# Performance work log

Measured on AMD Instinct MI355X. Metric: run time of the kernel, lower is better.

## Reference

```python
import jax, jax.numpy as jnp
import numpy as np

K = 4096      # kmer_num = 4^k with k=6
C = 10        # class_num
D = 128       # embedding dim
B = 1000      # batch of reads
L = 512       # kmers per read


def setup_inputs() -> dict:
    key = jax.random.key(0)
    k1, k2, k3, k4, k5 = jax.random.split(key, 5)
    u = jax.random.uniform(k1, (K, K))
    pair_counts = jnp.where(u > 0.9, jnp.floor(u * 50.0), 0.0).astype(jnp.float32)
    pair_counts = pair_counts * (1.0 - jnp.eye(K, dtype=jnp.float32))
    reads = jax.random.randint(k2, (B, L), 0, K, dtype=jnp.int32)
    read_labels = jax.random.randint(k3, (B,), 0, C, dtype=jnp.int32)
    embs = 2.0 * jax.random.uniform(k4, (K, D), dtype=jnp.float32) - 1.0
    softmax_weights = 2.0 * jax.random.uniform(k5, (C, D), dtype=jnp.float32) - 1.0
    delta = jnp.float32(0.5)
    return {"pair_counts": pair_counts, "reads": reads, "read_labels": read_labels,
            "delta": delta, "embs": embs, "softmax_weights": softmax_weights}


def reference(pair_counts, reads, read_labels, delta, embs, softmax_weights):
    # ---- supervised term: per-read bincount -> weighted emb sum -> log_softmax ----
    # counts[b, kmer] = number of occurrences of kmer in read b (batched bincount)
    counts = jnp.zeros((B, K), dtype=jnp.float32).at[
        jnp.arange(B)[:, None], reads].add(1.0)
    read_emb = counts @ embs                              # [B, D]
    logits = read_emb @ softmax_weights.T                 # [B, C]
    logp = jax.nn.log_softmax(logits, axis=1)             # [B, C]
    supervised = -jnp.sum(logp[jnp.arange(B), read_labels])

    # ---- unsupervised term: pairwise embedding distances over nonzero pairs ----
    sqn = jnp.sum(embs * embs, axis=1)                    # [K]
    sq = sqn[:, None] + sqn[None, :] - 2.0 * (embs @ embs.T)
    sq = jnp.maximum(sq, 0.0)                             # [K, K]
    mask = pair_counts != 0
    dist = jnp.sqrt(jnp.where(mask, sq, 1.0))             # safe sqrt off-edges
    rate = jnp.exp(-dist)
    # degrees * log(rate) - rate, with log(rate) = -dist, summed over nonzero pairs
    term = jnp.where(mask, -pair_counts * dist - rate, 0.0)
    scale = 1.0 / (np.float32(K) * np.float32(K))         # 1 / 4^(2k)
    unsupervised = -jnp.sum(term) * scale

    return delta * supervised + (1.0 - delta) * unsupervised
```

## Files before the change

kernel.cpp:

```cpp
#include <hip/hip_runtime.h>
#include <hip/hip_bf16.h>

#define KN 4096
#define CN 10
#define DN 128
#define BN 1000
#define LN 512
#define UB 4096

typedef float f32x4 __attribute__((ext_vector_type(4)));
typedef short bf16x8 __attribute__((ext_vector_type(8)));

__device__ __forceinline__ short bf16bits(float x) {
    __hip_bfloat16 h = __float2bfloat16(x);
    return *reinterpret_cast<short*>(&h);
}
__device__ __forceinline__ void gload_lds16(const float* g, void* l) {
    __builtin_amdgcn_global_load_lds(
        (const __attribute__((address_space(1))) void*)g,
        (__attribute__((address_space(3))) void*)l, 16, 0, 0);
}

__global__ __launch_bounds__(256) void w2v_prep(const float* __restrict__ embs,
                                                const float* __restrict__ W,
                                                float* __restrict__ sqn,
                                                short* __restrict__ ebf,
                                                float* __restrict__ P) {
    int blk = blockIdx.x, t = threadIdx.x;
    if (blk < 512) {
        int row = t >> 5, lane = t & 31;
        int r = blk * 8 + row;
        float4 v = ((const float4*)embs)[r * 32 + lane];
        short4 s4;
        s4.x = bf16bits(v.x); s4.y = bf16bits(v.y);
        s4.z = bf16bits(v.z); s4.w = bf16bits(v.w);
        ((short4*)ebf)[r * 32 + lane] = s4;
        float ss = v.x * v.x + v.y * v.y + v.z * v.z + v.w * v.w;
        #pragma unroll
        for (int m = 16; m >= 1; m >>= 1) ss += __shfl_xor(ss, m, 64);
        if (lane == 0) sqn[r] = ss;
        return;
    }
    int pb = blk - 512;
    int r = pb * 64 + (t >> 2);
    int q = t & 3;
    const float4* er = (const float4*)(embs + (size_t)r * DN) + q * 8;
    const float4* w4 = (const float4*)W;
    float s[CN];
    #pragma unroll
    for (int c = 0; c < CN; ++c) s[c] = 0.f;
    #pragma unroll
    for (int d4 = 0; d4 < 8; ++d4) {
        float4 e = er[d4];
        #pragma unroll
        for (int c = 0; c < CN; ++c) {
            float4 w = w4[c * 32 + q * 8 + d4];
            s[c] += e.x * w.x + e.y * w.y + e.z * w.z + e.w * w.w;
        }
    }
    #pragma unroll
    for (int c = 0; c < CN; ++c) {
        s[c] += __shfl_xor(s[c], 1, 64);
        s[c] += __shfl_xor(s[c], 2, 64);
    }
    if (q == 0) {
        float* pr = P + (size_t)r * 12;
        #pragma unroll
        for (int c = 0; c < CN; ++c) pr[c] = s[c];
        pr[10] = 0.f; pr[11] = 0.f;
    }
}

__global__ __launch_bounds__(64) void w2v_main(const short* __restrict__ ebf,
                                               const float* __restrict__ sqn,
                                               const float* __restrict__ pc,
                                               const float* __restrict__ P,
                                               const int* __restrict__ reads,
                                               const int* __restrict__ labels,
                                               float* __restrict__ psup,
                                               float* __restrict__ puns) {
    __shared__ char pcT[16 * 1040];
    int blk = blockIdx.x, t = threadIdx.x;

    if (blk < UB) {
        int i0 = (blk >> 5) * 32;
        int j0 = (blk & 31) * 128;
        int lr = t & 15, lg = t >> 4;

        const short* Arow = ebf + (size_t)(i0 + lr) * DN;
        const short* Brow = ebf + (size_t)(j0 + lr) * DN;

        f32x4 acc4[2][8];
        #pragma unroll
        for (int mi = 0; mi < 2; ++mi)
            #pragma unroll
            for (int nj = 0; nj < 8; ++nj)
                acc4[mi][nj] = (f32x4){0.f, 0.f, 0.f, 0.f};

        #pragma unroll
        for (int kk = 0; kk < 4; ++kk) {
            int ko = kk * 32 + lg * 8;
            bf16x8 a0 = *(const bf16x8*)(Arow + ko);
            bf16x8 a1 = *(const bf16x8*)(Arow + (size_t)16 * DN + ko);
            bf16x8 bfr[8];
            #pragma unroll
            for (int nj = 0; nj < 8; ++nj)
                bfr[nj] = *(const bf16x8*)(Brow + (size_t)nj * 16 * DN + ko);
            #pragma unroll
            for (int nj = 0; nj < 8; ++nj) {
                acc4[0][nj] = __builtin_amdgcn_mfma_f32_16x16x32_bf16(
                    a0, bfr[nj], acc4[0][nj], 0, 0, 0);
                acc4[1][nj] = __builtin_amdgcn_mfma_f32_16x16x32_bf16(
                    a1, bfr[nj], acc4[1][nj], 0, 0, 0);
            }
        }
        __builtin_amdgcn_sched_barrier(0);

        float siv[8], sjv[8];
        #pragma unroll
        for (int mi = 0; mi < 2; ++mi)
            #pragma unroll
            for (int v = 0; v < 4; ++v)
                siv[mi * 4 + v] = sqn[i0 + mi * 16 + lg * 4 + v];
        #pragma unroll
        for (int nj = 0; nj < 8; ++nj) sjv[nj] = sqn[j0 + nj * 16 + lr];
        __builtin_amdgcn_sched_barrier(0);

        int rsub = t >> 5, csub = t & 31;
        #pragma unroll
        for (int p = 0; p < 16; ++p) {
            const float* src = pc + (size_t)(i0 + 2 * p + rsub) * KN + j0 + csub * 4;
            gload_lds16(src, pcT + p * 1040);
        }
        __builtin_amdgcn_sched_barrier(0);

        float part = 0.f;
        #pragma unroll
        for (int mi = 0; mi < 2; ++mi) {
            if (mi == 0) { asm volatile("s_waitcnt vmcnt(8)" ::: "memory"); }
            else         { asm volatile("s_waitcnt vmcnt(0)" ::: "memory"); }
            __builtin_amdgcn_sched_barrier(0);
            #pragma unroll
            for (int v = 0; v < 4; ++v) {
                int row = mi * 16 + lg * 4 + v;
                const float* prow =
                    (const float*)(pcT + (row >> 1) * 1040 + (row & 1) * 512);
                float si = siv[mi * 4 + v];
                #pragma unroll
                for (int nj = 0; nj < 8; ++nj) {
                    float pp = prow[nj * 16 + lr];
                    float sq = fmaxf(si + sjv[nj] - 2.f * acc4[mi][nj][v], 0.f);
                    float dd = sqrtf(sq);
                    float tt = fmaf(pp, dd, __expf(-dd));
                    part += (pp != 0.f) ? tt : 0.f;
                }
            }
        }
        #pragma unroll
        for (int off = 32; off > 0; off >>= 1) part += __shfl_down(part, off, 64);
        if (t == 0) puns[blk] = part;
        return;
    }

    int b = blk - UB;
    const int4* rr = (const int4*)(reads + (size_t)b * LN);
    int4 r0 = rr[t * 2], r1 = rr[t * 2 + 1];
    int idx[8] = { r0.x, r0.y, r0.z, r0.w, r1.x, r1.y, r1.z, r1.w };
    const float4* P4 = (const float4*)P;
    float s[12];
    #pragma unroll
    for (int i = 0; i < 12; ++i) s[i] = 0.f;
    #pragma unroll
    for (int k = 0; k < 8; ++k) {
        size_t o = (size_t)idx[k] * 3;
        float4 x = P4[o], y = P4[o + 1], z = P4[o + 2];
        s[0] += x.x; s[1] += x.y; s[2]  += x.z; s[3]  += x.w;
        s[4] += y.x; s[5] += y.y; s[6]  += y.z; s[7]  += y.w;
        s[8] += z.x; s[9] += z.y; s[10] += z.z; s[11] += z.w;
    }
    #pragma unroll
    for (int off = 32; off > 0; off >>= 1)
        #pragma unroll
        for (int i = 0; i < CN; ++i) s[i] += __shfl_down(s[i], off, 64);
    if (t == 0) {
        float m = s[0];
        #pragma unroll
        for (int c = 1; c < CN; ++c) m = fmaxf(m, s[c]);
        float se = 0.f;
        #pragma unroll
        for (int c = 0; c < CN; ++c) se += __expf(s[c] - m);
        float lse = m + __logf(se);
        psup[b] = -(s[labels[b]] - lse);
    }
}

__global__ __launch_bounds__(256) void w2v_final(const float* __restrict__ psup,
                                                 const float* __restrict__ puns,
                                                 const float* __restrict__ delta,
                                                 float* __restrict__ out) {
    __shared__ float r1[4], r2[4];
    int t = threadIdx.x;
    float a = 0.f, bsum = 0.f;
    for (int i = t; i < BN; i += 256)   a += psup[i];
    for (int i = t; i < UB; i += 256)   bsum += puns[i];
    #pragma unroll
    for (int off = 32; off > 0; off >>= 1) {
        a += __shfl_down(a, off, 64);
        bsum += __shfl_down(bsum, off, 64);
    }
    int lane = t & 63, wave = t >> 6;
    if (lane == 0) { r1[wave] = a; r2[wave] = bsum; }
    __syncthreads();
    if (t == 0) {
        float sup = (r1[0] + r1[1]) + (r1[2] + r1[3]);
        float uns = ((r2[0] + r2[1]) + (r2[2] + r2[3])) * (1.f / 16777216.f);
        float d = delta[0];
        out[0] = d * sup + (1.f - d) * uns;
    }
}

extern "C" void kernel_launch(void* const* d_in, const int* in_sizes, int n_in,
                              void* d_out, int out_size, void* d_ws, size_t ws_size,
                              hipStream_t stream) {
    const float* pc     = (const float*)d_in[0];
    const int*   reads  = (const int*)  d_in[1];
    const int*   labels = (const int*)  d_in[2];
    const float* delta  = (const float*)d_in[3];
    const float* embs   = (const float*)d_in[4];
    const float* W      = (const float*)d_in[5];
    float* out = (float*)d_out;

    char* ws = (char*)d_ws;
    float* sqn  = (float*)ws;
    float* P    = (float*)(ws + 16384);
    short* ebf  = (short*)(ws + 212992);
    float* psup = (float*)(ws + 1261568);
    float* puns = (float*)(ws + 1265664);

    w2v_prep<<<576, 256, 0, stream>>>(embs, W, sqn, ebf, P);
    w2v_main<<<UB + BN, 64, 0, stream>>>(ebf, sqn, pc, P, reads, labels, psup, puns);
    w2v_final<<<1, 256, 0, stream>>>(psup, puns, delta, out);
}
```

Before: 56.08 us.

## Make pair-distance blocks persistent over column chunks with triple-buffered LDS prefetch

Each unsupervised block now keeps its 32-row A fragments in registers and loops over 16 column chunks of 64 instead of handling one 32x128 tile. The pair_counts tiles stream into LDS through a three-buffer rotation with an XOR swizzle, so the next loads overlap the MFMA and epilogue work. The aim is to cut block count and launch/tail overhead, reuse A across chunks, and hide global-memory latency. The cost is fewer blocks (512) and less parallelism to hide latency, and the chunk loop now runs serially within each block.

```diff
diff --git a/kernel.cpp b/kernel.cpp
--- a/kernel.cpp
+++ b/kernel.cpp
@@ -6,7 +6,7 @@
 #define DN 128
 #define BN 1000
 #define LN 512
-#define UB 4096
+#define UB2 512
 
 typedef float f32x4 __attribute__((ext_vector_type(4)));
 typedef short bf16x8 __attribute__((ext_vector_type(8)));
@@ -79,82 +79,111 @@
                                                const int* __restrict__ labels,
                                                float* __restrict__ psup,
                                                float* __restrict__ puns) {
-    __shared__ char pcT[16 * 1040];
+    __shared__ char buf0[8192], buf1[8192], buf2[8192];
     int blk = blockIdx.x, t = threadIdx.x;
 
-    if (blk < UB) {
-        int i0 = (blk >> 5) * 32;
-        int j0 = (blk & 31) * 128;
+    if (blk < UB2) {
+        int i0 = (blk >> 2) * 32;
+        int jb = (blk & 3) * 1024;
         int lr = t & 15, lg = t >> 4;
-
-        const short* Arow = ebf + (size_t)(i0 + lr) * DN;
-        const short* Brow = ebf + (size_t)(j0 + lr) * DN;
-
-        f32x4 acc4[2][8];
-        #pragma unroll
-        for (int mi = 0; mi < 2; ++mi)
-            #pragma unroll
-            for (int nj = 0; nj < 8; ++nj)
-                acc4[mi][nj] = (f32x4){0.f, 0.f, 0.f, 0.f};
-
+        int drow = t >> 4;
+        int dcol = (t & 15) * 4;
+
+        const short* Ar = ebf + (size_t)(i0 + lr) * DN;
+        bf16x8 afr[4][2];
         #pragma unroll
         for (int kk = 0; kk < 4; ++kk) {
-            int ko = kk * 32 + lg * 8;
-            bf16x8 a0 = *(const bf16x8*)(Arow + ko);
-            bf16x8 a1 = *(const bf16x8*)(Arow + (size_t)16 * DN + ko);
-            bf16x8 bfr[8];
-            #pragma unroll
-            for (int nj = 0; nj < 8; ++nj)
-                bfr[nj] = *(const bf16x8*)(Brow + (size_t)nj * 16 * DN + ko);
-            #pragma unroll
-            for (int nj = 0; nj < 8; ++nj) {
-                acc4[0][nj] = __builtin_amdgcn_mfma_f32_16x16x32_bf16(
-                    a0, bfr[nj], acc4[0][nj], 0, 0, 0);
-                acc4[1][nj] = __builtin_amdgcn_mfma_f32_16x16x32_bf16(
-                    a1, bfr[nj], acc4[1][nj], 0, 0, 0);
-            }
-        }
-        __builtin_amdgcn_sched_barrier(0);
-
-        float siv[8], sjv[8];
+            afr[kk][0] = *(const bf16x8*)(Ar + kk * 32 + lg * 8);
+            afr[kk][1] = *(const bf16x8*)(Ar + 16 * DN + kk * 32 + lg * 8);
+        }
+        float siv[8];
         #pragma unroll
         for (int mi = 0; mi < 2; ++mi)
             #pragma unroll
             for (int v = 0; v < 4; ++v)
                 siv[mi * 4 + v] = sqn[i0 + mi * 16 + lg * 4 + v];
-        #pragma unroll
-        for (int nj = 0; nj < 8; ++nj) sjv[nj] = sqn[j0 + nj * 16 + lr];
         __builtin_amdgcn_sched_barrier(0);
 
-        int rsub = t >> 5, csub = t & 31;
-        #pragma unroll
-        for (int p = 0; p < 16; ++p) {
-            const float* src = pc + (size_t)(i0 + 2 * p + rsub) * KN + j0 + csub * 4;
-            gload_lds16(src, pcT + p * 1040);
+        char* d0 = buf0; char* d1 = buf1; char* d2 = buf2;
+        #pragma unroll
+        for (int p = 0; p < 8; ++p) {
+            const float* s0 = pc + (size_t)(i0 + 4 * p + drow) * KN + jb
+                              + (dcol ^ ((p & 3) << 3));
+            gload_lds16(s0, d0 + p * 1024);
+        }
+        #pragma unroll
+        for (int p = 0; p < 8; ++p) {
+            const float* s1 = pc + (size_t)(i0 + 4 * p + drow) * KN + jb + 64
+                              + (dcol ^ ((p & 3) << 3));
+            gload_lds16(s1, d1 + p * 1024);
         }
         __builtin_amdgcn_sched_barrier(0);
 
         float part = 0.f;
-        #pragma unroll
-        for (int mi = 0; mi < 2; ++mi) {
-            if (mi == 0) { asm volatile("s_waitcnt vmcnt(8)" ::: "memory"); }
-            else         { asm volatile("s_waitcnt vmcnt(0)" ::: "memory"); }
-            __builtin_amdgcn_sched_barrier(0);
-            #pragma unroll
-            for (int v = 0; v < 4; ++v) {
-                int row = mi * 16 + lg * 4 + v;
-                const float* prow =
-                    (const float*)(pcT + (row >> 1) * 1040 + (row & 1) * 512);
-                float si = siv[mi * 4 + v];
-                #pragma unroll
-                for (int nj = 0; nj < 8; ++nj) {
-                    float pp = prow[nj * 16 + lr];
-                    float sq = fmaxf(si + sjv[nj] - 2.f * acc4[mi][nj][v], 0.f);
-                    float dd = sqrtf(sq);
-                    float tt = fmaf(pp, dd, __expf(-dd));
-                    part += (pp != 0.f) ? tt : 0.f;
+        for (int c = 0; c < 16; ++c) {
+            __builtin_amdgcn_sched_barrier(0);
+            int jc = jb + c * 64;
+            float sjv[4];
+            #pragma unroll
+            for (int nj = 0; nj < 4; ++nj) sjv[nj] = sqn[jc + nj * 16 + lr];
+            const short* Br = ebf + (size_t)(jc + lr) * DN;
+            bf16x8 bfr[4][4];
+            #pragma unroll
+            for (int kk = 0; kk < 4; ++kk)
+                #pragma unroll
+                for (int nj = 0; nj < 4; ++nj)
+                    bfr[kk][nj] = *(const bf16x8*)(Br + (size_t)nj * 16 * DN
+                                                   + kk * 32 + lg * 8);
+            __builtin_amdgcn_sched_barrier(0);
+            if (c < 14) {
+                int j2 = jc + 128;
+                #pragma unroll
+                for (int p = 0; p < 8; ++p) {
+                    const float* sp = pc + (size_t)(i0 + 4 * p + drow) * KN + j2
+                                      + (dcol ^ ((p & 3) << 3));
+                    gload_lds16(sp, d2 + p * 1024);
                 }
             }
+            __builtin_amdgcn_sched_barrier(0);
+            if (c < 14) { asm volatile("s_waitcnt vmcnt(8)" ::: "memory"); }
+            else        { asm volatile("s_waitcnt vmcnt(0)" ::: "memory"); }
+            __builtin_amdgcn_sched_barrier(0);
+
+            f32x4 acc[2][4];
+            #pragma unroll
+            for (int mi = 0; mi < 2; ++mi)
+                #pragma unroll
+                for (int nj = 0; nj < 4; ++nj)
+                    acc[mi][nj] = (f32x4){0.f, 0.f, 0.f, 0.f};
+            #pragma unroll
+            for (int kk = 0; kk < 4; ++kk)
+                #pragma unroll
+                for (int nj = 0; nj < 4; ++nj) {
+                    acc[0][nj] = __builtin_amdgcn_mfma_f32_16x16x32_bf16(
+                        afr[kk][0], bfr[kk][nj], acc[0][nj], 0, 0, 0);
+                    acc[1][nj] = __builtin_amdgcn_mfma_f32_16x16x32_bf16(
+                        afr[kk][1], bfr[kk][nj], acc[1][nj], 0, 0, 0);
+                }
+
+            #pragma unroll
+            for (int mi = 0; mi < 2; ++mi) {
+                #pragma unroll
+                for (int v = 0; v < 4; ++v) {
+                    int row = mi * 16 + lg * 4 + v;
+                    const char* rowp = d0 + row * 256;
+                    float si = siv[mi * 4 + v];
+                    #pragma unroll
+                    for (int nj = 0; nj < 4; ++nj) {
+                        float pp = *(const float*)(rowp +
+                                     ((nj * 64 + lr * 4) ^ (lg << 5)));
+                        float sq = fmaxf(si + sjv[nj] - 2.f * acc[mi][nj][v], 0.f);
+                        float dd = sqrtf(sq);
+                        float tt = fmaf(pp, dd, __expf(-dd));
+                        part += (pp != 0.f) ? tt : 0.f;
+                    }
+                }
+            }
+            char* tmp = d0; d0 = d1; d1 = d2; d2 = tmp;
         }
         #pragma unroll
         for (int off = 32; off > 0; off >>= 1) part += __shfl_down(part, off, 64);
@@ -162,7 +191,7 @@
         return;
     }
 
-    int b = blk - UB;
+    int b = blk - UB2;
     const int4* rr = (const int4*)(reads + (size_t)b * LN);
     int4 r0 = rr[t * 2], r1 = rr[t * 2 + 1];
     int idx[8] = { r0.x, r0.y, r0.z, r0.w, r1.x, r1.y, r1.z, r1.w };
@@ -202,7 +231,7 @@
     int t = threadIdx.x;
     float a = 0.f, bsum = 0.f;
     for (int i = t; i < BN; i += 256)   a += psup[i];
-    for (int i = t; i < UB; i += 256)   bsum += puns[i];
+    for (int i = t; i < UB2; i += 256)  bsum += puns[i];
     #pragma unroll
     for (int off = 32; off > 0; off >>= 1) {
         a += __shfl_down(a, off, 64);
@@ -238,6 +267,6 @@
     float* puns = (float*)(ws + 1265664);
 
     w2v_prep<<<576, 256, 0, stream>>>(embs, W, sqn, ebf, P);
-    w2v_main<<<UB + BN, 64, 0, stream>>>(ebf, sqn, pc, P, reads, labels, psup, puns);
+    w2v_main<<<UB2 + BN, 64, 0, stream>>>(ebf, sqn, pc, P, reads, labels, psup, puns);
     w2v_final<<<1, 256, 0, stream>>>(psup, puns, delta, out);
 }
```

After: 72.55 us. +29.4%, slower.

## Split fused gram+pair kernel into bf16 distance-matrix pass and streaming reduction

Applied to the files above, without the earlier changes.

Replaces the fused kernel, which computed 32x128 gram tiles and loaded pair counts into LDS, with two kernels. The first computes 128x128 gram tiles with 4 waves and writes sqrt distances to a bf16 K×K workspace matrix. The second streams pair_counts and the distance matrix with wide coalesced loads, applies the masked term, and shares its launch with the supervised per-read blocks. The split decouples MFMA work from the pair_counts stream, but adds a 32 MB write and read of the distance matrix, an extra launch, and bf16 rounding of the distances.

```diff
diff --git a/kernel.cpp b/kernel.cpp
--- a/kernel.cpp
+++ b/kernel.cpp
@@ -6,7 +6,7 @@
 #define DN 128
 #define BN 1000
 #define LN 512
-#define UB 4096
+#define SB 2048
 
 typedef float f32x4 __attribute__((ext_vector_type(4)));
 typedef short bf16x8 __attribute__((ext_vector_type(8)));
@@ -15,10 +15,13 @@
     __hip_bfloat16 h = __float2bfloat16(x);
     return *reinterpret_cast<short*>(&h);
 }
-__device__ __forceinline__ void gload_lds16(const float* g, void* l) {
-    __builtin_amdgcn_global_load_lds(
-        (const __attribute__((address_space(1))) void*)g,
-        (__attribute__((address_space(3))) void*)l, 16, 0, 0);
+__device__ __forceinline__ float bflo(unsigned u) {
+    unsigned v = u << 16;
+    return *reinterpret_cast<float*>(&v);
+}
+__device__ __forceinline__ float bfhi(unsigned u) {
+    unsigned v = u & 0xFFFF0000u;
+    return *reinterpret_cast<float*>(&v);
 }
 
 __global__ __launch_bounds__(256) void w2v_prep(const float* __restrict__ embs,
@@ -71,98 +74,128 @@
     }
 }
 
-__global__ __launch_bounds__(64) void w2v_main(const short* __restrict__ ebf,
-                                               const float* __restrict__ sqn,
-                                               const float* __restrict__ pc,
-                                               const float* __restrict__ P,
-                                               const int* __restrict__ reads,
-                                               const int* __restrict__ labels,
-                                               float* __restrict__ psup,
-                                               float* __restrict__ puns) {
-    __shared__ char pcT[16 * 1040];
+__global__ __launch_bounds__(256, 4) void w2v_gram(const short* __restrict__ ebf,
+                                                   const float* __restrict__ sqn,
+                                                   short* __restrict__ dmat) {
+    __shared__ short dl[128 * 128];
+    __shared__ float sqi[128];
+    __shared__ float sqj[128];
+
+    int t  = threadIdx.x;
+    int i0 = blockIdx.y * 128;
+    int j0 = blockIdx.x * 128;
+
+    if (t < 128) sqi[t] = sqn[i0 + t];
+    else         sqj[t - 128] = sqn[j0 + t - 128];
+
+    int wave = t >> 6, lane = t & 63;
+    int wr = (wave >> 1) * 64;
+    int wc = (wave & 1) * 64;
+    int lr = lane & 15;
+    int lg = lane >> 4;
+
+    const short* Ai = ebf + (size_t)(i0 + wr + lr) * DN;
+    const short* Bj = ebf + (size_t)(j0 + wc + lr) * DN;
+
+    f32x4 acc4[4][4];
+    #pragma unroll
+    for (int mi = 0; mi < 4; ++mi)
+        #pragma unroll
+        for (int nj = 0; nj < 4; ++nj)
+            acc4[mi][nj] = (f32x4){0.f, 0.f, 0.f, 0.f};
+
+    #pragma unroll
+    for (int kk = 0; kk < 4; ++kk) {
+        int ko = kk * 32 + lg * 8;
+        bf16x8 afr[4], bfr[4];
+        #pragma unroll
+        for (int mi = 0; mi < 4; ++mi) {
+            afr[mi] = *(const bf16x8*)(Ai + (size_t)mi * 16 * DN + ko);
+            bfr[mi] = *(const bf16x8*)(Bj + (size_t)mi * 16 * DN + ko);
+        }
+        #pragma unroll
+        for (int mi = 0; mi < 4; ++mi)
+            #pragma unroll
+            for (int nj = 0; nj < 4; ++nj)
+                acc4[mi][nj] = __builtin_amdgcn_mfma_f32_16x16x32_bf16(
+                    afr[mi], bfr[nj], acc4[mi][nj], 0, 0, 0);
+    }
+
+    __syncthreads();
+
+    #pragma unroll
+    for (int mi = 0; mi < 4; ++mi) {
+        #pragma unroll
+        for (int v = 0; v < 4; ++v) {
+            int row = wr + 16 * mi + lg * 4 + v;
+            float si = sqi[row];
+            #pragma unroll
+            for (int nj = 0; nj < 4; ++nj) {
+                int col = wc + 16 * nj + lr;
+                float sq = fmaxf(si + sqj[col] - 2.f * acc4[mi][nj][v], 0.f);
+                dl[row * 128 + col] = bf16bits(sqrtf(sq));
+            }
+        }
+    }
+    __syncthreads();
+
+    const uint4* s4 = (const uint4*)dl;
+    #pragma unroll
+    for (int k = 0; k < 8; ++k) {
+        int idx  = k * 256 + t;
+        int row  = idx >> 4;
+        int colq = idx & 15;
+        ((uint4*)(dmat + (size_t)(i0 + row) * KN + j0))[colq] = s4[idx];
+    }
+}
+
+__global__ __launch_bounds__(256) void w2v_stream(const float* __restrict__ pc,
+                                                  const short* __restrict__ dmat,
+                                                  const float* __restrict__ P,
+                                                  const int* __restrict__ reads,
+                                                  const int* __restrict__ labels,
+                                                  float* __restrict__ psup,
+                                                  float* __restrict__ puns) {
+    __shared__ float wred[4];
     int blk = blockIdx.x, t = threadIdx.x;
 
-    if (blk < UB) {
-        int i0 = (blk >> 5) * 32;
-        int j0 = (blk & 31) * 128;
-        int lr = t & 15, lg = t >> 4;
-
-        const short* Arow = ebf + (size_t)(i0 + lr) * DN;
-        const short* Brow = ebf + (size_t)(j0 + lr) * DN;
-
-        f32x4 acc4[2][8];
-        #pragma unroll
-        for (int mi = 0; mi < 2; ++mi)
+    if (blk < SB) {
+        float4 pa[4], pb[4];
+        uint4  dv[4];
+        #pragma unroll
+        for (int it = 0; it < 4; ++it) {
+            size_t q = ((size_t)(it * SB + blk)) * 256 + t;
+            pa[it] = ((const float4*)pc)[2 * q];
+            pb[it] = ((const float4*)pc)[2 * q + 1];
+            dv[it] = ((const uint4*)dmat)[q];
+        }
+        float part = 0.f;
+        #pragma unroll
+        for (int it = 0; it < 4; ++it) {
+            float p[8] = { pa[it].x, pa[it].y, pa[it].z, pa[it].w,
+                           pb[it].x, pb[it].y, pb[it].z, pb[it].w };
+            float d[8] = { bflo(dv[it].x), bfhi(dv[it].x),
+                           bflo(dv[it].y), bfhi(dv[it].y),
+                           bflo(dv[it].z), bfhi(dv[it].z),
+                           bflo(dv[it].w), bfhi(dv[it].w) };
             #pragma unroll
-            for (int nj = 0; nj < 8; ++nj)
-                acc4[mi][nj] = (f32x4){0.f, 0.f, 0.f, 0.f};
-
-        #pragma unroll
-        for (int kk = 0; kk < 4; ++kk) {
-            int ko = kk * 32 + lg * 8;
-            bf16x8 a0 = *(const bf16x8*)(Arow + ko);
-            bf16x8 a1 = *(const bf16x8*)(Arow + (size_t)16 * DN + ko);
-            bf16x8 bfr[8];
-            #pragma unroll
-            for (int nj = 0; nj < 8; ++nj)
-                bfr[nj] = *(const bf16x8*)(Brow + (size_t)nj * 16 * DN + ko);
-            #pragma unroll
-            for (int nj = 0; nj < 8; ++nj) {
-                acc4[0][nj] = __builtin_amdgcn_mfma_f32_16x16x32_bf16(
-                    a0, bfr[nj], acc4[0][nj], 0, 0, 0);
-                acc4[1][nj] = __builtin_amdgcn_mfma_f32_16x16x32_bf16(
-                    a1, bfr[nj], acc4[1][nj], 0, 0, 0);
+            for (int e = 0; e < 8; ++e) {
+                float tt = fmaf(p[e], d[e], __expf(-d[e]));
+                part += (p[e] != 0.f) ? tt : 0.f;
             }
         }
-        __builtin_amdgcn_sched_barrier(0);
-
-        float siv[8], sjv[8];
-        #pragma unroll
-        for (int mi = 0; mi < 2; ++mi)
-            #pragma unroll
-            for (int v = 0; v < 4; ++v)
-                siv[mi * 4 + v] = sqn[i0 + mi * 16 + lg * 4 + v];
-        #pragma unroll
-        for (int nj = 0; nj < 8; ++nj) sjv[nj] = sqn[j0 + nj * 16 + lr];
-        __builtin_amdgcn_sched_barrier(0);
-
-        int rsub = t >> 5, csub = t & 31;
-        #pragma unroll
-        for (int p = 0; p < 16; ++p) {
-            const float* src = pc + (size_t)(i0 + 2 * p + rsub) * KN + j0 + csub * 4;
-            gload_lds16(src, pcT + p * 1040);
-        }
-        __builtin_amdgcn_sched_barrier(0);
-
-        float part = 0.f;
-        #pragma unroll
-        for (int mi = 0; mi < 2; ++mi) {
-            if (mi == 0) { asm volatile("s_waitcnt vmcnt(8)" ::: "memory"); }
-            else         { asm volatile("s_waitcnt vmcnt(0)" ::: "memory"); }
-            __builtin_amdgcn_sched_barrier(0);
-            #pragma unroll
-            for (int v = 0; v < 4; ++v) {
-                int row = mi * 16 + lg * 4 + v;
-                const float* prow =
-                    (const float*)(pcT + (row >> 1) * 1040 + (row & 1) * 512);
-                float si = siv[mi * 4 + v];
-                #pragma unroll
-                for (int nj = 0; nj < 8; ++nj) {
-                    float pp = prow[nj * 16 + lr];
-                    float sq = fmaxf(si + sjv[nj] - 2.f * acc4[mi][nj][v], 0.f);
-                    float dd = sqrtf(sq);
-                    float tt = fmaf(pp, dd, __expf(-dd));
-                    part += (pp != 0.f) ? tt : 0.f;
-                }
-            }
-        }
         #pragma unroll
         for (int off = 32; off > 0; off >>= 1) part += __shfl_down(part, off, 64);
-        if (t == 0) puns[blk] = part;
+        int lane = t & 63, wave = t >> 6;
+        if (lane == 0) wred[wave] = part;
+        __syncthreads();
+        if (t == 0)
+            puns[blk] = (wred[0] + wred[1]) + (wred[2] + wred[3]);
         return;
     }
 
-    int b = blk - UB;
+    if (t >= 64) return;
+    int b = blk - SB;
     const int4* rr = (const int4*)(reads + (size_t)b * LN);
     int4 r0 = rr[t * 2], r1 = rr[t * 2 + 1];
     int idx[8] = { r0.x, r0.y, r0.z, r0.w, r1.x, r1.y, r1.z, r1.w };
@@ -201,8 +234,8 @@
     __shared__ float r1[4], r2[4];
     int t = threadIdx.x;
     float a = 0.f, bsum = 0.f;
-    for (int i = t; i < BN; i += 256)   a += psup[i];
-    for (int i = t; i < UB; i += 256)   bsum += puns[i];
+    for (int i = t; i < BN; i += 256)  a += psup[i];
+    for (int i = t; i < SB; i += 256)  bsum += puns[i];
     #pragma unroll
     for (int off = 32; off > 0; off >>= 1) {
         a += __shfl_down(a, off, 64);
@@ -236,8 +269,10 @@
     short* ebf  = (short*)(ws + 212992);
     float* psup = (float*)(ws + 1261568);
     float* puns = (float*)(ws + 1265664);
+    short* dmat = (short*)(ws + 1277952);
 
     w2v_prep<<<576, 256, 0, stream>>>(embs, W, sqn, ebf, P);
-    w2v_main<<<UB + BN, 64, 0, stream>>>(ebf, sqn, pc, P, reads, labels, psup, puns);
+    w2v_gram<<<dim3(32, 32), 256, 0, stream>>>(ebf, sqn, dmat);
+    w2v_stream<<<SB + BN, 256, 0, stream>>>(pc, dmat, P, reads, labels, psup, puns);
     w2v_final<<<1, 256, 0, stream>>>(psup, puns, delta, out);
 }
```

Measured after the change: 68.86 us. 22.8% more time.

## Use 256-thread blocks with 32x512 distance tiles and block-wide read reduction

Applied to the files above, without the earlier changes.

The pairwise-distance kernel moves from 4096 single-wave blocks (32x128 tiles) to 1024 four-wave blocks, each covering a 32x512 tile. The block stages the full 32x512 pair-count slab into LDS up front with a padded row stride, and each wave computes its own 128-column MFMA subtile. Read blocks now use 256 threads with one gather pair per thread and a two-stage shuffle plus LDS reduction. This cuts launch and per-block overhead and the number of partial sums, but swaps the fine-grained vmcnt overlap for a block-wide __syncthreads and uses much more LDS per block.

```diff
diff --git a/kernel.cpp b/kernel.cpp
--- a/kernel.cpp
+++ b/kernel.cpp
@@ -6,7 +6,8 @@
 #define DN 128
 #define BN 1000
 #define LN 512
-#define UB 4096
+#define UBN 1024
+#define RSTRIDE 2064
 
 typedef float f32x4 __attribute__((ext_vector_type(4)));
 typedef short bf16x8 __attribute__((ext_vector_type(8)));
@@ -71,50 +72,62 @@
     }
 }
 
-__global__ __launch_bounds__(64) void w2v_main(const short* __restrict__ ebf,
-                                               const float* __restrict__ sqn,
-                                               const float* __restrict__ pc,
-                                               const float* __restrict__ P,
-                                               const int* __restrict__ reads,
-                                               const int* __restrict__ labels,
-                                               float* __restrict__ psup,
-                                               float* __restrict__ puns) {
-    __shared__ char pcT[16 * 1040];
+struct MainSm { char pcL[32 * RSTRIDE]; float wred[4]; };
+struct SupSm  { int sidx[LN]; float wredS[4][12]; float slog[CN]; };
+union K2Sm { MainSm m; SupSm s; };
+
+__global__ __launch_bounds__(256, 2) void w2v_main(const short* __restrict__ ebf,
+                                                   const float* __restrict__ sqn,
+                                                   const float* __restrict__ pc,
+                                                   const float* __restrict__ P,
+                                                   const int* __restrict__ reads,
+                                                   const int* __restrict__ labels,
+                                                   float* __restrict__ psup,
+                                                   float* __restrict__ puns) {
+    __shared__ K2Sm sm;
     int blk = blockIdx.x, t = threadIdx.x;
 
-    if (blk < UB) {
-        int i0 = (blk >> 5) * 32;
-        int j0 = (blk & 31) * 128;
-        int lr = t & 15, lg = t >> 4;
-
-        const short* Arow = ebf + (size_t)(i0 + lr) * DN;
-        const short* Brow = ebf + (size_t)(j0 + lr) * DN;
-
-        f32x4 acc4[2][8];
+    if (blk < UBN) {
+        int i0 = (blk >> 3) * 32;
+        int j0 = (blk & 7) * 512;
+        int w = t >> 6, lane = t & 63;
+        int lr = lane & 15, lg = lane >> 4;
+
+        #pragma unroll
+        for (int p = 0; p < 8; ++p) {
+            int r = 8 * w + p;
+            const float* srow = pc + (size_t)(i0 + r) * KN + j0 + lane * 4;
+            char* drow = sm.m.pcL + r * RSTRIDE;
+            gload_lds16(srow,       drow);
+            gload_lds16(srow + 256, drow + 1024);
+        }
+        __builtin_amdgcn_sched_barrier(0);
+
+        const short* Ar = ebf + (size_t)(i0 + lr) * DN;
+        const short* Br = ebf + (size_t)(j0 + w * 128 + lr) * DN;
+        f32x4 acc[2][8];
         #pragma unroll
         for (int mi = 0; mi < 2; ++mi)
             #pragma unroll
             for (int nj = 0; nj < 8; ++nj)
-                acc4[mi][nj] = (f32x4){0.f, 0.f, 0.f, 0.f};
-
+                acc[mi][nj] = (f32x4){0.f, 0.f, 0.f, 0.f};
         #pragma unroll
         for (int kk = 0; kk < 4; ++kk) {
             int ko = kk * 32 + lg * 8;
-            bf16x8 a0 = *(const bf16x8*)(Arow + ko);
-            bf16x8 a1 = *(const bf16x8*)(Arow + (size_t)16 * DN + ko);
+            bf16x8 a0 = *(const bf16x8*)(Ar + ko);
+            bf16x8 a1 = *(const bf16x8*)(Ar + 16 * DN + ko);
             bf16x8 bfr[8];
             #pragma unroll
             for (int nj = 0; nj < 8; ++nj)
-                bfr[nj] = *(const bf16x8*)(Brow + (size_t)nj * 16 * DN + ko);
+                bfr[nj] = *(const bf16x8*)(Br + (size_t)nj * 16 * DN + ko);
             #pragma unroll
             for (int nj = 0; nj < 8; ++nj) {
-                acc4[0][nj] = __builtin_amdgcn_mfma_f32_16x16x32_bf16(
-                    a0, bfr[nj], acc4[0][nj], 0, 0, 0);
-                acc4[1][nj] = __builtin_amdgcn_mfma_f32_16x16x32_bf16(
-                    a1, bfr[nj], acc4[1][nj], 0, 0, 0);
+                acc[0][nj] = __builtin_amdgcn_mfma_f32_16x16x32_bf16(
+                    a0, bfr[nj], acc[0][nj], 0, 0, 0);
+                acc[1][nj] = __builtin_amdgcn_mfma_f32_16x16x32_bf16(
+                    a1, bfr[nj], acc[1][nj], 0, 0, 0);
             }
         }
-        __builtin_amdgcn_sched_barrier(0);
 
         float siv[8], sjv[8];
         #pragma unroll
@@ -123,33 +136,24 @@
             for (int v = 0; v < 4; ++v)
                 siv[mi * 4 + v] = sqn[i0 + mi * 16 + lg * 4 + v];
         #pragma unroll
-        for (int nj = 0; nj < 8; ++nj) sjv[nj] = sqn[j0 + nj * 16 + lr];
-        __builtin_amdgcn_sched_barrier(0);
-
-        int rsub = t >> 5, csub = t & 31;
-        #pragma unroll
-        for (int p = 0; p < 16; ++p) {
-            const float* src = pc + (size_t)(i0 + 2 * p + rsub) * KN + j0 + csub * 4;
-            gload_lds16(src, pcT + p * 1040);
-        }
-        __builtin_amdgcn_sched_barrier(0);
+        for (int nj = 0; nj < 8; ++nj)
+            sjv[nj] = sqn[j0 + w * 128 + nj * 16 + lr];
+
+        __syncthreads();
 
         float part = 0.f;
         #pragma unroll
         for (int mi = 0; mi < 2; ++mi) {
-            if (mi == 0) { asm volatile("s_waitcnt vmcnt(8)" ::: "memory"); }
-            else         { asm volatile("s_waitcnt vmcnt(0)" ::: "memory"); }
-            __builtin_amdgcn_sched_barrier(0);
             #pragma unroll
             for (int v = 0; v < 4; ++v) {
                 int row = mi * 16 + lg * 4 + v;
-                const float* prow =
-                    (const float*)(pcT + (row >> 1) * 1040 + (row & 1) * 512);
+                const char* rowp = sm.m.pcL + row * RSTRIDE;
                 float si = siv[mi * 4 + v];
                 #pragma unroll
                 for (int nj = 0; nj < 8; ++nj) {
-                    float pp = prow[nj * 16 + lr];
-                    float sq = fmaxf(si + sjv[nj] - 2.f * acc4[mi][nj][v], 0.f);
+                    int colf = w * 128 + nj * 16 + lr;
+                    float pp = *(const float*)(rowp + colf * 4);
+                    float sq = fmaxf(si + sjv[nj] - 2.f * acc[mi][nj][v], 0.f);
                     float dd = sqrtf(sq);
                     float tt = fmaf(pp, dd, __expf(-dd));
                     part += (pp != 0.f) ? tt : 0.f;
@@ -158,39 +162,46 @@
         }
         #pragma unroll
         for (int off = 32; off > 0; off >>= 1) part += __shfl_down(part, off, 64);
-        if (t == 0) puns[blk] = part;
+        if (lane == 0) sm.m.wred[w] = part;
+        __syncthreads();
+        if (t == 0)
+            puns[blk] = (sm.m.wred[0] + sm.m.wred[1]) + (sm.m.wred[2] + sm.m.wred[3]);
         return;
     }
 
-    int b = blk - UB;
-    const int4* rr = (const int4*)(reads + (size_t)b * LN);
-    int4 r0 = rr[t * 2], r1 = rr[t * 2 + 1];
-    int idx[8] = { r0.x, r0.y, r0.z, r0.w, r1.x, r1.y, r1.z, r1.w };
+    int b = blk - UBN;
+    for (int i = t; i < LN; i += 256) sm.s.sidx[i] = reads[b * LN + i];
+    __syncthreads();
     const float4* P4 = (const float4*)P;
-    float s[12];
-    #pragma unroll
-    for (int i = 0; i < 12; ++i) s[i] = 0.f;
-    #pragma unroll
-    for (int k = 0; k < 8; ++k) {
-        size_t o = (size_t)idx[k] * 3;
-        float4 x = P4[o], y = P4[o + 1], z = P4[o + 2];
-        s[0] += x.x; s[1] += x.y; s[2]  += x.z; s[3]  += x.w;
-        s[4] += y.x; s[5] += y.y; s[6]  += y.z; s[7]  += y.w;
-        s[8] += z.x; s[9] += z.y; s[10] += z.z; s[11] += z.w;
-    }
+    size_t o0 = (size_t)sm.s.sidx[t] * 3;
+    size_t o1 = (size_t)sm.s.sidx[t + 256] * 3;
+    float4 a0 = P4[o0], b0 = P4[o0 + 1], c0 = P4[o0 + 2];
+    float4 a1 = P4[o1], b1 = P4[o1 + 1], c1 = P4[o1 + 2];
+    float s[12] = { a0.x + a1.x, a0.y + a1.y, a0.z + a1.z, a0.w + a1.w,
+                    b0.x + b1.x, b0.y + b1.y, b0.z + b1.z, b0.w + b1.w,
+                    c0.x + c1.x, c0.y + c1.y, c0.z + c1.z, c0.w + c1.w };
     #pragma unroll
     for (int off = 32; off > 0; off >>= 1)
         #pragma unroll
-        for (int i = 0; i < CN; ++i) s[i] += __shfl_down(s[i], off, 64);
+        for (int i = 0; i < 12; ++i) s[i] += __shfl_down(s[i], off, 64);
+    int lane = t & 63, wave = t >> 6;
+    if (lane == 0)
+        #pragma unroll
+        for (int i = 0; i < 12; ++i) sm.s.wredS[wave][i] = s[i];
+    __syncthreads();
+    if (t < CN)
+        sm.s.slog[t] = sm.s.wredS[0][t] + sm.s.wredS[1][t]
+                     + sm.s.wredS[2][t] + sm.s.wredS[3][t];
+    __syncthreads();
     if (t == 0) {
-        float m = s[0];
-        #pragma unroll
-        for (int c = 1; c < CN; ++c) m = fmaxf(m, s[c]);
+        float m = sm.s.slog[0];
+        #pragma unroll
+        for (int c = 1; c < CN; ++c) m = fmaxf(m, sm.s.slog[c]);
         float se = 0.f;
         #pragma unroll
-        for (int c = 0; c < CN; ++c) se += __expf(s[c] - m);
+        for (int c = 0; c < CN; ++c) se += __expf(sm.s.slog[c] - m);
         float lse = m + __logf(se);
-        psup[b] = -(s[labels[b]] - lse);
+        psup[b] = -(sm.s.slog[labels[b]] - lse);
     }
 }
 
@@ -202,7 +213,7 @@
     int t = threadIdx.x;
     float a = 0.f, bsum = 0.f;
     for (int i = t; i < BN; i += 256)   a += psup[i];
-    for (int i = t; i < UB; i += 256)   bsum += puns[i];
+    for (int i = t; i < UBN; i += 256)  bsum += puns[i];
     #pragma unroll
     for (int off = 32; off > 0; off >>= 1) {
         a += __shfl_down(a, off, 64);
@@ -238,6 +249,6 @@
     float* puns = (float*)(ws + 1265664);
 
     w2v_prep<<<576, 256, 0, stream>>>(embs, W, sqn, ebf, P);
-    w2v_main<<<UB + BN, 64, 0, stream>>>(ebf, sqn, pc, P, reads, labels, psup, puns);
+    w2v_main<<<UBN + BN, 256, 0, stream>>>(ebf, sqn, pc, P, reads, labels, psup, puns);
     w2v_final<<<1, 256, 0, stream>>>(psup, puns, delta, out);
 }
```

New measurement: 60.39 us. 7.7% more time.
